# Optimization experiments

Measured on AMD Instinct MI355X. Metric: run time of the kernel, lower is better.

Reference implementation:

```python
import jax, jax.numpy as jnp
import numpy as np

B = 65536          # users in batch
N_USERS = 200000
N_ENTITY = 100000
D = 64             # n_factors
N_RK = 3
LEAKY_SLOPE = 0.2


def setup_inputs() -> dict:
    key = jax.random.key(0)
    ks = jax.random.split(key, 8)
    rng = np.random.default_rng(0)
    # ragged lengths per user (>=1 so no empty segments)
    len_a = rng.integers(1, 80, size=B)
    len_c = rng.integers(1, 20, size=B)
    seg_a = jnp.asarray(np.repeat(np.arange(B), len_a), dtype=jnp.int32)
    seg_c = jnp.asarray(np.repeat(np.arange(B), len_c), dtype=jnp.int32)
    Ta, Tc = int(len_a.sum()), int(len_c.sum())
    return {
        "user_id": jax.random.randint(ks[0], (B,), 0, N_USERS),
        "artists_ids": jax.random.randint(ks[1], (Ta,), 0, N_ENTITY),
        "artists_seg": seg_a,
        "categories_ids": jax.random.randint(ks[2], (Tc,), 0, N_ENTITY),
        "categories_seg": seg_c,
        "user_factors": jax.random.normal(ks[3], (N_USERS, D), dtype=jnp.float32),
        "entity_factors": jax.random.normal(ks[4], (N_ENTITY, D), dtype=jnp.float32),
        "relation_k": jax.random.normal(ks[5], (D, N_RK), dtype=jnp.float32),
    }


def reference(user_id, artists_ids, artists_seg, categories_ids, categories_seg,
              user_factors, entity_factors, relation_k):
    users = user_factors[user_id]                                  # [B, D]
    # aspect importance: leaky_relu(U @ Rk) -> softmax over n_rk
    scores = jax.nn.softmax(
        jax.nn.leaky_relu(users @ relation_k, LEAKY_SLOPE), axis=1)  # [B, 3]

    def contrib(ids, seg):
        # ragged gather + per-item dot + segment mean (== calculate_score)
        d = jnp.einsum('td,td->t', entity_factors[ids], users[seg])  # [T]
        s = jax.ops.segment_sum(d, seg, num_segments=B)
        cnt = jax.ops.segment_sum(jnp.ones_like(d), seg, num_segments=B)
        return s / cnt

    c_a = contrib(artists_ids, artists_seg)        # contribute_actors [B]
    c_c = contrib(categories_ids, categories_seg)  # contribute_directors [B]

    s_a, s_c = scores[:, 0], scores[:, 1]
    prediction = (c_a * s_a + c_c * s_c) / (s_a + s_c)
    return (prediction, scores, c_a, c_c)
```

## Files before the change

kernel.cpp:

```cpp
#include <hip/hip_runtime.h>

#define NB 65536
#define D 64
#define SLOPE 0.2f

typedef _Float16 h2f __attribute__((ext_vector_type(2)));

__device__ __forceinline__ h2f as_h2(unsigned x) {
    union { unsigned u; h2f h; } v; v.u = x; return v.h;
}

struct UH { h2f h0, h1, h2, h3; };

__device__ __forceinline__ float dot8(uint4 w, const UH& u, float acc) {
#if __has_builtin(__builtin_amdgcn_fdot2)
    acc = __builtin_amdgcn_fdot2(as_h2(w.x), u.h0, acc, false);
    acc = __builtin_amdgcn_fdot2(as_h2(w.y), u.h1, acc, false);
    acc = __builtin_amdgcn_fdot2(as_h2(w.z), u.h2, acc, false);
    acc = __builtin_amdgcn_fdot2(as_h2(w.w), u.h3, acc, false);
#else
    h2f t0 = as_h2(w.x) * u.h0 + as_h2(w.y) * u.h1;
    h2f t1 = as_h2(w.z) * u.h2 + as_h2(w.w) * u.h3;
    acc += (float)t0.x + (float)t0.y + (float)t1.x + (float)t1.y;
#endif
    return acc;
}

__device__ __forceinline__ float reduce8(float v) {
#pragma unroll
    for (int off = 1; off <= 4; off <<= 1)
        v += __shfl_xor(v, off, 64);
    return v;
}
__device__ __forceinline__ float reduce64(float v) {
#pragma unroll
    for (int off = 1; off <= 32; off <<= 1)
        v += __shfl_xor(v, off, 64);
    return v;
}

__device__ __forceinline__ int lower_bound(const int* __restrict__ seg, int n, int key) {
    int lo = 0, hi = n;
    while (lo < hi) {
        int mid = (lo + hi) >> 1;
        if (seg[mid] < key) lo = mid + 1;
        else hi = mid;
    }
    return lo;
}

__global__ __launch_bounds__(256)
void prepass(const float2* __restrict__ ef2, unsigned* __restrict__ eh, int n2,
             const int* __restrict__ a_seg, int Ta, int* __restrict__ offs_a,
             const int* __restrict__ c_seg, int Tc, int* __restrict__ offs_c)
{
    const int t = blockIdx.x * blockDim.x + threadIdx.x;
    if (t < n2) {
        float2 v = ef2[t];
        h2f h = { (_Float16)v.x, (_Float16)v.y };
        union { h2f h; unsigned u; } cv; cv.h = h;
        eh[t] = cv.u;
    }
    if (t < Ta) {
        int s = a_seg[t];
        if (t == 0) offs_a[0] = 0;
        else if (a_seg[t - 1] != s) offs_a[s] = t;
        if (t == Ta - 1) offs_a[s + 1] = Ta;
    }
    if (t < Tc) {
        int s = c_seg[t];
        if (t == 0) offs_c[0] = 0;
        else if (c_seg[t - 1] != s) offs_c[s] = t;
        if (t == Tc - 1) offs_c[s + 1] = Tc;
    }
}

__global__ __launch_bounds__(256)
void aspect_fused(const int* __restrict__ user_id,
                  const int* __restrict__ a_ids, const int* __restrict__ offs_a,
                  const int* __restrict__ c_ids, const int* __restrict__ offs_c,
                  const float* __restrict__ user_factors,
                  const uint4* __restrict__ efh,
                  const float* __restrict__ relation_k,
                  float* __restrict__ out)
{
    const int b    = blockIdx.x * 4 + (threadIdx.x >> 6);
    const int lane = threadIdx.x & 63;
    const int r = lane >> 3;
    const int c = lane & 7;

    const int uid = user_id[b];
    const float4 ua = reinterpret_cast<const float4*>(user_factors)[uid * 16 + 2 * c];
    const float4 ub = reinterpret_cast<const float4*>(user_factors)[uid * 16 + 2 * c + 1];

    float p0 = 0.f, p1 = 0.f, p2 = 0.f;
    {
        const float uv[8] = {ua.x, ua.y, ua.z, ua.w, ub.x, ub.y, ub.z, ub.w};
#pragma unroll
        for (int j = 0; j < 8; ++j) {
            const int row = 8 * c + j;
            p0 += uv[j] * relation_k[row * 3 + 0];
            p1 += uv[j] * relation_k[row * 3 + 1];
            p2 += uv[j] * relation_k[row * 3 + 2];
        }
    }
    float l0 = reduce8(p0), l1 = reduce8(p1), l2 = reduce8(p2);
    l0 = l0 > 0.f ? l0 : SLOPE * l0;
    l1 = l1 > 0.f ? l1 : SLOPE * l1;
    l2 = l2 > 0.f ? l2 : SLOPE * l2;
    const float m  = fmaxf(l0, fmaxf(l1, l2));
    const float e0 = __expf(l0 - m);
    const float e1 = __expf(l1 - m);
    const float e2 = __expf(l2 - m);
    const float inv = 1.0f / (e0 + e1 + e2);
    const float s0 = e0 * inv, s1 = e1 * inv, s2 = e2 * inv;

    const int sa = offs_a[b], ea = offs_a[b + 1];
    const int sc = offs_c[b], ec = offs_c[b + 1];
    const int na = ea - sa;
    const int nc = ec - sc;
    const int n  = na + nc;

    UH uh;
    uh.h0 = h2f{ (_Float16)ua.x, (_Float16)ua.y };
    uh.h1 = h2f{ (_Float16)ua.z, (_Float16)ua.w };
    uh.h2 = h2f{ (_Float16)ub.x, (_Float16)ub.y };
    uh.h3 = h2f{ (_Float16)ub.z, (_Float16)ub.w };

    float accA = 0.f, accC = 0.f;
    for (int t = 0; t < n; t += 32) {
#pragma unroll
        for (int jj = 0; jj < 4; ++jj) {
            const int i = t + 8 * jj + r;
            if (i < n) {
                const bool isA = i < na;
                const int id = isA ? a_ids[sa + i] : c_ids[sc + i - na];
                const uint4 w = efh[id * 8 + c];
                const float d = dot8(w, uh, 0.f);
                accA += isA ? d : 0.f;
                accC += isA ? 0.f : d;
            }
        }
    }

    const float c_a = reduce64(accA) / (float)na;
    const float c_c = reduce64(accC) / (float)nc;

    const float pred = (c_a * s0 + c_c * s1) / (s0 + s1);

    if (lane == 0) {
        out[b]          = pred;
        out[4 * NB + b] = c_a;
        out[5 * NB + b] = c_c;
    }
    if (lane < 3) {
        const float sv = (lane == 0) ? s0 : ((lane == 1) ? s1 : s2);
        out[NB + 3 * b + lane] = sv;
    }
}

__global__ __launch_bounds__(256)
void aspect_fallback(const int* __restrict__ user_id,
                     const int* __restrict__ a_ids, const int* __restrict__ a_seg, int Ta,
                     const int* __restrict__ c_ids, const int* __restrict__ c_seg, int Tc,
                     const float* __restrict__ user_factors,
                     const float4* __restrict__ ef4,
                     const float* __restrict__ relation_k,
                     float* __restrict__ out)
{
    const int b    = blockIdx.x * 4 + (threadIdx.x >> 6);
    const int lane = threadIdx.x & 63;
    const int g = lane >> 4, k = lane & 15;

    const int uid = user_id[b];
    const float4 u4 = reinterpret_cast<const float4*>(user_factors)[uid * 16 + k];

    float p0 = 0.f, p1 = 0.f, p2 = 0.f;
    {
        const float uv[4] = {u4.x, u4.y, u4.z, u4.w};
#pragma unroll
        for (int j = 0; j < 4; ++j) {
            const int row = 4 * k + j;
            p0 += uv[j] * relation_k[row * 3 + 0];
            p1 += uv[j] * relation_k[row * 3 + 1];
            p2 += uv[j] * relation_k[row * 3 + 2];
        }
    }
#pragma unroll
    for (int off = 1; off <= 8; off <<= 1) {
        p0 += __shfl_xor(p0, off, 64);
        p1 += __shfl_xor(p1, off, 64);
        p2 += __shfl_xor(p2, off, 64);
    }
    float l0 = p0 > 0.f ? p0 : SLOPE * p0;
    float l1 = p1 > 0.f ? p1 : SLOPE * p1;
    float l2 = p2 > 0.f ? p2 : SLOPE * p2;
    const float m  = fmaxf(l0, fmaxf(l1, l2));
    const float e0 = __expf(l0 - m), e1 = __expf(l1 - m), e2 = __expf(l2 - m);
    const float inv = 1.0f / (e0 + e1 + e2);
    const float s0 = e0 * inv, s1 = e1 * inv, s2 = e2 * inv;

    auto gd = [&](const int* __restrict__ ids, int s, int e) -> float {
        float ax = 0.f, ay = 0.f, az = 0.f, aw = 0.f;
        int t = s;
        for (; t + 4 <= e; t += 4) {
            const float4 v0 = ef4[ids[t + g] * 16 + k];
            ax += v0.x; ay += v0.y; az += v0.z; aw += v0.w;
        }
        if (t + g < e) {
            const float4 v0 = ef4[ids[t + g] * 16 + k];
            ax += v0.x; ay += v0.y; az += v0.z; aw += v0.w;
        }
        return reduce64(ax * u4.x + ay * u4.y + az * u4.z + aw * u4.w);
    };

    const int sa = lower_bound(a_seg, Ta, b), ea = lower_bound(a_seg, Ta, b + 1);
    const int sc = lower_bound(c_seg, Tc, b), ec = lower_bound(c_seg, Tc, b + 1);
    const float c_a = gd(a_ids, sa, ea) / (float)(ea - sa);
    const float c_c = gd(c_ids, sc, ec) / (float)(ec - sc);
    const float pred = (c_a * s0 + c_c * s1) / (s0 + s1);

    if (lane == 0) {
        out[b]          = pred;
        out[4 * NB + b] = c_a;
        out[5 * NB + b] = c_c;
    }
    if (lane < 3) {
        const float sv = (lane == 0) ? s0 : ((lane == 1) ? s1 : s2);
        out[NB + 3 * b + lane] = sv;
    }
}

extern "C" void kernel_launch(void* const* d_in, const int* in_sizes, int n_in,
                              void* d_out, int out_size, void* d_ws, size_t ws_size,
                              hipStream_t stream) {
    const int*   user_id        = (const int*)d_in[0];
    const int*   artists_ids    = (const int*)d_in[1];
    const int*   artists_seg    = (const int*)d_in[2];
    const int*   categories_ids = (const int*)d_in[3];
    const int*   categories_seg = (const int*)d_in[4];
    const float* user_factors   = (const float*)d_in[5];
    const float* entity_factors = (const float*)d_in[6];
    const float* relation_k     = (const float*)d_in[7];
    float* out = (float*)d_out;

    const int Ta = in_sizes[1];
    const int Tc = in_sizes[3];
    const int n_ent_elems = in_sizes[6];
    const int n2 = n_ent_elems / 2;

    const size_t table_bytes = (size_t)n_ent_elems * 2;
    const size_t offs_bytes  = (size_t)2 * (NB + 1) * sizeof(int);

    if (ws_size >= table_bytes + offs_bytes) {
        unsigned* efh    = (unsigned*)d_ws;
        int*      offs_a = (int*)((unsigned char*)d_ws + table_bytes);
        int*      offs_c = offs_a + (NB + 1);
        int prep_n = n2 > Ta ? n2 : Ta;
        if (Tc > prep_n) prep_n = Tc;
        prepass<<<(prep_n + 255) / 256, 256, 0, stream>>>(
            (const float2*)entity_factors, efh, n2,
            artists_seg, Ta, offs_a,
            categories_seg, Tc, offs_c);
        aspect_fused<<<NB / 4, 256, 0, stream>>>(user_id,
            artists_ids, offs_a, categories_ids, offs_c,
            user_factors, (const uint4*)efh, relation_k, out);
    } else {
        aspect_fallback<<<NB / 4, 256, 0, stream>>>(user_id,
            artists_ids, artists_seg, Ta,
            categories_ids, categories_seg, Tc,
            user_factors, (const float4*)entity_factors, relation_k, out);
    }
}
```

Measured before the change: 88.93 us.

## Prefetch segment ids and entity rows into registers before computing dots

The main kernel now reads the segment offsets and the item ids early and issues every entity-row gather for up to 10 artist groups and 3 category groups into register arrays before doing any dot products. Artist and category items are handled in separate loops instead of one merged loop with a per-item select. The goal is more memory-level parallelism, so gather latency overlaps with the softmax math instead of being serialised in the loop. In exchange register use goes up, which may lower occupancy, and long segments fall back to a serial tail loop.

Result: faster. 78.40 us (-11.8%).

```diff
diff --git a/kernel.cpp b/kernel.cpp
--- a/kernel.cpp
+++ b/kernel.cpp
@@ -3,6 +3,8 @@
 #define NB 65536
 #define D 64
 #define SLOPE 0.2f
+#define GA 10
+#define GC 3
 
 typedef _Float16 h2f __attribute__((ext_vector_type(2)));
 
@@ -76,13 +78,13 @@
 }
 
 __global__ __launch_bounds__(256)
-void aspect_fused(const int* __restrict__ user_id,
-                  const int* __restrict__ a_ids, const int* __restrict__ offs_a,
-                  const int* __restrict__ c_ids, const int* __restrict__ offs_c,
-                  const float* __restrict__ user_factors,
-                  const uint4* __restrict__ efh,
-                  const float* __restrict__ relation_k,
-                  float* __restrict__ out)
+void aspect_deep(const int* __restrict__ user_id,
+                 const int* __restrict__ a_ids, const int* __restrict__ offs_a,
+                 const int* __restrict__ c_ids, const int* __restrict__ offs_c,
+                 const float* __restrict__ user_factors,
+                 const uint4* __restrict__ efh,
+                 const float* __restrict__ relation_k,
+                 float* __restrict__ out)
 {
     const int b    = blockIdx.x * 4 + (threadIdx.x >> 6);
     const int lane = threadIdx.x & 63;
@@ -92,6 +94,20 @@
     const int uid = user_id[b];
     const float4 ua = reinterpret_cast<const float4*>(user_factors)[uid * 16 + 2 * c];
     const float4 ub = reinterpret_cast<const float4*>(user_factors)[uid * 16 + 2 * c + 1];
+
+    const int sa = offs_a[b], ea = offs_a[b + 1];
+    const int sc = offs_c[b], ec = offs_c[b + 1];
+    const int na = ea - sa, nc = ec - sc;
+    const int Ga = (na + 7) >> 3;
+    const int Gc = (nc + 7) >> 3;
+
+    int ida[GA], idc[GC];
+#pragma unroll
+    for (int g = 0; g < GA; ++g)
+        if (g < Ga) ida[g] = a_ids[sa + min(8 * g + r, na - 1)];
+#pragma unroll
+    for (int g = 0; g < GC; ++g)
+        if (g < Gc) idc[g] = c_ids[sc + min(8 * g + r, nc - 1)];
 
     float p0 = 0.f, p1 = 0.f, p2 = 0.f;
     {
@@ -115,33 +131,38 @@
     const float inv = 1.0f / (e0 + e1 + e2);
     const float s0 = e0 * inv, s1 = e1 * inv, s2 = e2 * inv;
 
-    const int sa = offs_a[b], ea = offs_a[b + 1];
-    const int sc = offs_c[b], ec = offs_c[b + 1];
-    const int na = ea - sa;
-    const int nc = ec - sc;
-    const int n  = na + nc;
-
     UH uh;
     uh.h0 = h2f{ (_Float16)ua.x, (_Float16)ua.y };
     uh.h1 = h2f{ (_Float16)ua.z, (_Float16)ua.w };
     uh.h2 = h2f{ (_Float16)ub.x, (_Float16)ub.y };
     uh.h3 = h2f{ (_Float16)ub.z, (_Float16)ub.w };
 
+    uint4 wa[GA], wc[GC];
+#pragma unroll
+    for (int g = 0; g < GA; ++g)
+        if (g < Ga) wa[g] = efh[(unsigned)ida[g] * 8 + c];
+#pragma unroll
+    for (int g = 0; g < GC; ++g)
+        if (g < Gc) wc[g] = efh[(unsigned)idc[g] * 8 + c];
+
     float accA = 0.f, accC = 0.f;
-    for (int t = 0; t < n; t += 32) {
-#pragma unroll
-        for (int jj = 0; jj < 4; ++jj) {
-            const int i = t + 8 * jj + r;
-            if (i < n) {
-                const bool isA = i < na;
-                const int id = isA ? a_ids[sa + i] : c_ids[sc + i - na];
-                const uint4 w = efh[id * 8 + c];
-                const float d = dot8(w, uh, 0.f);
-                accA += isA ? d : 0.f;
-                accC += isA ? 0.f : d;
-            }
-        }
-    }
+#pragma unroll
+    for (int g = 0; g < GA; ++g)
+        if (g < Ga) {
+            const float d = dot8(wa[g], uh, 0.f);
+            accA += (8 * g + r < na) ? d : 0.f;
+        }
+#pragma unroll
+    for (int g = 0; g < GC; ++g)
+        if (g < Gc) {
+            const float d = dot8(wc[g], uh, 0.f);
+            accC += (8 * g + r < nc) ? d : 0.f;
+        }
+
+    for (int i = 8 * GA + r; i < na; i += 8)
+        accA = dot8(efh[(unsigned)a_ids[sa + i] * 8 + c], uh, accA);
+    for (int i = 8 * GC + r; i < nc; i += 8)
+        accC = dot8(efh[(unsigned)c_ids[sc + i] * 8 + c], uh, accC);
 
     const float c_a = reduce64(accA) / (float)na;
     const float c_c = reduce64(accC) / (float)nc;
@@ -262,7 +283,7 @@
             (const float2*)entity_factors, efh, n2,
             artists_seg, Ta, offs_a,
             categories_seg, Tc, offs_c);
-        aspect_fused<<<NB / 4, 256, 0, stream>>>(user_id,
+        aspect_deep<<<NB / 4, 256, 0, stream>>>(user_id,
             artists_ids, offs_a, categories_ids, offs_c,
             user_factors, (const uint4*)efh, relation_k, out);
     } else {
```
